# Performance work log

Hardware: AMD Instinct MI355X
Metric: run time of the kernel (lower is better)

The kernel has to match this reference:

```python
import jax, jax.numpy as jnp
import numpy as np

EMBED_DIM = 768
NUM_HEADS = 12
HEAD_DIM = EMBED_DIM // NUM_HEADS


def setup_inputs() -> dict:
    key = jax.random.key(0)
    k_x, k_wqkv, k_bqkv, k_wp, k_bp = jax.random.split(key, 5)
    B, N, C = 2, 2048, EMBED_DIM
    lim_qkv = 1.0 / np.sqrt(C)
    lim_p = 1.0 / np.sqrt(C)
    return {
        "x": jax.random.normal(k_x, (B, N, C), dtype=jnp.float32),
        # torch Linear weights: [out_features, in_features]
        "w_qkv": jax.random.uniform(k_wqkv, (3 * C, C), minval=-lim_qkv, maxval=lim_qkv, dtype=jnp.float32),
        "b_qkv": jax.random.uniform(k_bqkv, (3 * C,), minval=-lim_qkv, maxval=lim_qkv, dtype=jnp.float32),
        "w_proj": jax.random.uniform(k_wp, (C, C), minval=-lim_p, maxval=lim_p, dtype=jnp.float32),
        "b_proj": jax.random.uniform(k_bp, (C,), minval=-lim_p, maxval=lim_p, dtype=jnp.float32),
    }


def reference(x, w_qkv, b_qkv, w_proj, b_proj):
    b, n, c = x.shape
    h, d = NUM_HEADS, HEAD_DIM
    qkv = x @ w_qkv.T + b_qkv                      # [b, n, 3c]
    qkv = qkv.reshape(b, n, 3, h, d).transpose(2, 0, 3, 1, 4)  # [3, b, h, n, d]
    q, k, v = qkv[0], qkv[1], qkv[2]
    scale = d ** -0.5
    attn = jnp.einsum('bhnd,bhmd->bhnm', q, k) * scale  # [b, h, n, n]
    attn = jax.nn.softmax(attn, axis=-1)
    # dropout is identity at inference (eval mode)
    out = jnp.einsum('bhnm,bhmd->bhnd', attn, v)        # [b, h, n, d]
    out = out.transpose(0, 2, 1, 3).reshape(b, n, c)    # [b, n, c]
    return out @ w_proj.T + b_proj
```

## Files before the change

### kernel.cpp

```cpp
#include <hip/hip_runtime.h>
#include <cstdint>
#include <cstddef>

using u16    = uint16_t;
using u16x4  = __attribute__((ext_vector_type(4))) uint16_t;
using u16x8  = __attribute__((ext_vector_type(8))) uint16_t;
using bf16x2 = __attribute__((ext_vector_type(2))) __bf16;
using bf16x8 = __attribute__((ext_vector_type(8))) __bf16;
using f32x4  = __attribute__((ext_vector_type(4))) float;

__device__ __forceinline__ u16 f2b(float f) {
    union { float f; uint32_t u; } x; x.f = f;
    uint32_t r = x.u + 0x7FFFu + ((x.u >> 16) & 1u);
    return (u16)(r >> 16);
}
__device__ __forceinline__ uint32_t pk2(float a, float b) {
    bf16x2 t; t[0] = (__bf16)a; t[1] = (__bf16)b;
    return __builtin_bit_cast(uint32_t, t);
}
__device__ __forceinline__ bf16x8 ld8(const u16* p) {
    union { u16x8 v; u16x4 h[2]; } r;
    r.h[0] = *(const u16x4*)p;
    r.h[1] = *(const u16x4*)(p + 4);
    return __builtin_bit_cast(bf16x8, r.v);
}
__device__ __forceinline__ void st8(u16* p, u16x8 v) {
    union { u16x8 v; u16x4 h[2]; } r; r.v = v;
    *(u16x4*)p       = r.h[0];
    *(u16x4*)(p + 4) = r.h[1];
}

__device__ __forceinline__ void load16_async(const u16* g, u16* lds_base) {
    __builtin_amdgcn_global_load_lds(
        (const __attribute__((address_space(1))) u16*)g,
        (__attribute__((address_space(3))) u16*)(uint32_t)(uintptr_t)lds_base,
        16, 0, 0);
}

__global__ void conv_k(const float* __restrict__ x,  u16* __restrict__ xb,  int nx4,
                       const float* __restrict__ w1, u16* __restrict__ w1b, int n14,
                       const float* __restrict__ w2, u16* __restrict__ w2b, int n24)
{
    const int t   = blockIdx.x * blockDim.x + threadIdx.x;
    const int stp = gridDim.x * blockDim.x;
    for (int i = t; i < nx4; i += stp) {
        f32x4 v = ((const f32x4*)x)[i];
        u16x4 o;
        #pragma unroll
        for (int e = 0; e < 4; e++) o[e] = f2b(v[e]);
        ((u16x4*)xb)[i] = o;
    }
    for (int i = t; i < n14; i += stp) {
        f32x4 v = ((const f32x4*)w1)[i];
        u16x4 o;
        #pragma unroll
        for (int e = 0; e < 4; e++) o[e] = f2b(v[e]);
        ((u16x4*)w1b)[i] = o;
    }
    for (int i = t; i < n24; i += stp) {
        f32x4 v = ((const f32x4*)w2)[i];
        u16x4 o;
        #pragma unroll
        for (int e = 0; e < 4; e++) o[e] = f2b(v[e]);
        ((u16x4*)w2b)[i] = o;
    }
}

__global__ __launch_bounds__(256, 2) void gemm_qkv(
    const u16* __restrict__ A, const u16* __restrict__ W,
    const float* __restrict__ bias,
    u16* __restrict__ O0, u16* __restrict__ O1, u16* __restrict__ O2)
{
    __shared__ alignas(16) u16 As[128 * 32];
    __shared__ alignas(16) u16 Bs[128 * 32];
    const int tid  = threadIdx.x;
    const int wid  = tid >> 6, lane = tid & 63;
    const int quad = lane >> 4, lc = lane & 15;
    const int row0 = blockIdx.x * 128, col0 = blockIdx.y * 128;
    const int wm   = (wid >> 1) * 64, wn = (wid & 1) * 64;

    const int srA = wid * 32 + (lane >> 2);
    const int scA = (lane & 3) * 8;

    f32x4 acc[4][4] = {};

    for (int k0 = 0; k0 < 768; k0 += 32) {
        __syncthreads();
        #pragma unroll
        for (int t = 0; t < 2; t++) {
            load16_async(&A[(row0 + srA + t*16) * 768 + k0 + scA], &As[wid*1024 + t*512]);
            load16_async(&W[(col0 + srA + t*16) * 768 + k0 + scA], &Bs[wid*1024 + t*512]);
        }
        __syncthreads();

        bf16x8 a[4], b[4];
        #pragma unroll
        for (int i = 0; i < 4; i++)
            a[i] = __builtin_bit_cast(bf16x8, *(const u16x8*)&As[(wm + i*16 + lc)*32 + quad*8]);
        #pragma unroll
        for (int j = 0; j < 4; j++)
            b[j] = __builtin_bit_cast(bf16x8, *(const u16x8*)&Bs[(wn + j*16 + lc)*32 + quad*8]);
        #pragma unroll
        for (int i = 0; i < 4; i++)
            #pragma unroll
            for (int j = 0; j < 4; j++)
                acc[i][j] = __builtin_amdgcn_mfma_f32_16x16x32_bf16(a[i], b[j], acc[i][j], 0, 0, 0);
    }

    #pragma unroll
    for (int i = 0; i < 4; i++) {
        #pragma unroll
        for (int j = 0; j < 4; j++) {
            const int gc = col0 + wn + j*16 + lc;
            const float bv = bias[gc];
            #pragma unroll
            for (int r = 0; r < 4; r++) {
                const int gr = row0 + wm + i*16 + quad*4 + r;
                const u16 ob = f2b(acc[i][j][r] + bv);
                const int which = gc / 768;
                const int c2 = gc - which * 768;
                if (which == 0)      O0[gr * 768 + c2] = ob;
                else if (which == 1) O1[gr * 768 + c2] = ob;
                else {
                    const int hh = c2 >> 6, dd = c2 & 63;
                    const int bb = gr >> 11, nn = gr & 2047;
                    O2[((bb*12 + hh)*64 + dd)*2048 + nn] = ob;
                }
            }
        }
    }
}

__global__ __launch_bounds__(256, 4) void gemm_proj(
    const u16* __restrict__ A, const u16* __restrict__ W,
    const float* __restrict__ bias, float* __restrict__ F0)
{
    __shared__ alignas(16) u16 As[64 * 32];
    __shared__ alignas(16) u16 Bs[64 * 32];
    const int tid  = threadIdx.x;
    const int wid  = tid >> 6, lane = tid & 63;
    const int quad = lane >> 4, lc = lane & 15;
    const int row0 = blockIdx.x * 64, col0 = blockIdx.y * 64;
    const int wm   = (wid >> 1) * 32, wn = (wid & 1) * 32;

    const int srA = wid * 16 + (lane >> 2);
    const int scA = (lane & 3) * 8;

    f32x4 acc[2][2] = {};

    for (int k0 = 0; k0 < 768; k0 += 32) {
        __syncthreads();
        load16_async(&A[(row0 + srA) * 768 + k0 + scA], &As[wid*512]);
        load16_async(&W[(col0 + srA) * 768 + k0 + scA], &Bs[wid*512]);
        __syncthreads();

        bf16x8 a[2], b[2];
        #pragma unroll
        for (int i = 0; i < 2; i++)
            a[i] = __builtin_bit_cast(bf16x8, *(const u16x8*)&As[(wm + i*16 + lc)*32 + quad*8]);
        #pragma unroll
        for (int j = 0; j < 2; j++)
            b[j] = __builtin_bit_cast(bf16x8, *(const u16x8*)&Bs[(wn + j*16 + lc)*32 + quad*8]);
        #pragma unroll
        for (int i = 0; i < 2; i++)
            #pragma unroll
            for (int j = 0; j < 2; j++)
                acc[i][j] = __builtin_amdgcn_mfma_f32_16x16x32_bf16(a[i], b[j], acc[i][j], 0, 0, 0);
    }

    #pragma unroll
    for (int i = 0; i < 2; i++)
        #pragma unroll
        for (int j = 0; j < 2; j++) {
            const int gc = col0 + wn + j*16 + lc;
            const float bv = bias[gc];
            #pragma unroll
            for (int r = 0; r < 4; r++) {
                const int gr = row0 + wm + i*16 + quad*4 + r;
                F0[gr * 768 + gc] = acc[i][j][r] + bv;
            }
        }
}

__global__ __launch_bounds__(256, 2) void attn_k(
    const u16* __restrict__ Q, const u16* __restrict__ K,
    const u16* __restrict__ V, u16* __restrict__ O)
{
    __shared__ alignas(16) char lds[53760];
    u16* Ks = (u16*)(lds);
    u16* Vs = (u16*)(lds + 17408);
    u16* Ps = (u16*)(lds + 35328);
    float* Obuf = (float*)(lds);
    float* Lbuf = (float*)(lds + 35328);

    const int tid  = threadIdx.x;
    const int wid  = tid >> 6, lane = tid & 63;
    const int quad = lane >> 4, lc = lane & 15;
    const int li = blockIdx.x;
    const int bh = li >> 5, qt = li & 31;
    const int b = bh / 12, h = bh - b * 12;
    const int q0 = qt * 64;

    const u16* Qp = Q + ((size_t)b * 2048) * 768 + h * 64;
    const u16* Kp = K + ((size_t)b * 2048) * 768 + h * 64;
    const u16* Vp = V + (size_t)bh * 64 * 2048;
    u16*       Op = O + ((size_t)b * 2048) * 768 + h * 64;

    bf16x8 qf[4][2];
    #pragma unroll
    for (int qg = 0; qg < 4; qg++)
        #pragma unroll
        for (int kb = 0; kb < 2; kb++) {
            u16x8 t = *(const u16x8*)&Qp[(q0 + qg*16 + lc) * 768 + kb*32 + quad*8];
            bf16x8 sc;
            #pragma unroll
            for (int e = 0; e < 8; e++) {
                union { uint32_t u; float f; } z; z.u = ((uint32_t)t[e]) << 16;
                sc[e] = (__bf16)(z.f * 0.125f);
            }
            qf[qg][kb] = sc;
        }

    float l_[4] = {};
    f32x4 o_[4][4] = {};

    const int kr = tid >> 3, kseg = (tid & 7) * 8;
    const int vr = tid >> 4, vseg = (tid & 15) * 8;
    const int kb0 = wid * 32;

    u16x8 kpre[4], vpre[4];
    #pragma unroll
    for (int p = 0; p < 4; p++)
        kpre[p] = *(const u16x8*)&Kp[(kr + p*32)*768 + kseg];
    #pragma unroll
    for (int p = 0; p < 4; p++)
        vpre[p] = *(const u16x8*)&Vp[(vr + p*16)*2048 + vseg];

    for (int kt = 0; kt < 16; kt++) {
        __syncthreads();
        #pragma unroll
        for (int p = 0; p < 4; p++)
            st8(&Ks[(kr + p*32)*68 + kseg], kpre[p]);
        #pragma unroll
        for (int p = 0; p < 4; p++)
            st8(&Vs[(vr + p*16)*140 + vseg], vpre[p]);
        __syncthreads();

        if (kt < 15) {
            #pragma unroll
            for (int p = 0; p < 4; p++)
                kpre[p] = *(const u16x8*)&Kp[((kt+1)*128 + kr + p*32)*768 + kseg];
            #pragma unroll
            for (int p = 0; p < 4; p++)
                vpre[p] = *(const u16x8*)&Vp[(vr + p*16)*2048 + (kt+1)*128 + vseg];
        }

        f32x4 s[2][4] = {};
        #pragma unroll
        for (int g = 0; g < 2; g++) {
            bf16x8 k0f = ld8(&Ks[(kb0 + g*16 + lc)*68 + quad*8]);
            bf16x8 k1f = ld8(&Ks[(kb0 + g*16 + lc)*68 + 32 + quad*8]);
            #pragma unroll
            for (int qg = 0; qg < 4; qg++) {
                s[g][qg] = __builtin_amdgcn_mfma_f32_16x16x32_bf16(k0f, qf[qg][0], s[g][qg], 0, 0, 0);
                s[g][qg] = __builtin_amdgcn_mfma_f32_16x16x32_bf16(k1f, qf[qg][1], s[g][qg], 0, 0, 0);
            }
        }

        #pragma unroll
        for (int g = 0; g < 2; g++)
            #pragma unroll
            for (int qg = 0; qg < 4; qg++)
                #pragma unroll
                for (int r = 0; r < 4; r++) {
                    float p = __expf(s[g][qg][r]);
                    s[g][qg][r] = p;
                    l_[qg] += p;
                }

        #pragma unroll
        for (int g = 0; g < 2; g++)
            #pragma unroll
            for (int qg = 0; qg < 4; qg++) {
                uint2 w;
                w.x = pk2(s[g][qg][0], s[g][qg][1]);
                w.y = pk2(s[g][qg][2], s[g][qg][3]);
                *(uint2*)&Ps[(wid*64 + qg*16 + lc)*36 + g*16 + quad*4] = w;
            }

        bf16x8 pf[4], vf[4];
        #pragma unroll
        for (int qg = 0; qg < 4; qg++)
            pf[qg] = ld8(&Ps[(wid*64 + qg*16 + lc)*36 + quad*8]);
        #pragma unroll
        for (int dg = 0; dg < 4; dg++)
            vf[dg] = ld8(&Vs[(dg*16 + lc)*140 + kb0 + quad*8]);
        #pragma unroll
        for (int dg = 0; dg < 4; dg++)
            #pragma unroll
            for (int qg = 0; qg < 4; qg++)
                o_[dg][qg] = __builtin_amdgcn_mfma_f32_16x16x32_bf16(vf[dg], pf[qg], o_[dg][qg], 0, 0, 0);
    }

    #pragma unroll
    for (int qg = 0; qg < 4; qg++) {
        l_[qg] += __shfl_xor(l_[qg], 16);
        l_[qg] += __shfl_xor(l_[qg], 32);
    }
    __syncthreads();
    if (quad == 0)
        #pragma unroll
        for (int qg = 0; qg < 4; qg++)
            Lbuf[wid*64 + qg*16 + lc] = l_[qg];
    __syncthreads();

    const int eq = tid & 63;
    const int ed = (tid >> 6) * 8;
    const float linv = 1.0f / (Lbuf[0*64 + eq] + Lbuf[1*64 + eq] +
                               Lbuf[2*64 + eq] + Lbuf[3*64 + eq]);

    #pragma unroll
    for (int dh = 0; dh < 2; dh++) {
        __syncthreads();
        #pragma unroll
        for (int b2 = 0; b2 < 2; b2++) {
            const int dg = dh*2 + b2;
            #pragma unroll
            for (int qg = 0; qg < 4; qg++)
                #pragma unroll
                for (int r = 0; r < 4; r++)
                    Obuf[(wid*32 + b2*16 + quad*4 + r)*64 + qg*16 + lc] = o_[dg][qg][r];
        }
        __syncthreads();
        u16x8 ov;
        #pragma unroll
        for (int j = 0; j < 8; j++) {
            const float sum = Obuf[(0*32 + ed + j)*64 + eq] + Obuf[(1*32 + ed + j)*64 + eq] +
                              Obuf[(2*32 + ed + j)*64 + eq] + Obuf[(3*32 + ed + j)*64 + eq];
            ov[j] = f2b(sum * linv);
        }
        *(u16x8*)&Op[(size_t)(q0 + eq) * 768 + dh*32 + ed] = ov;
    }
}

extern "C" void kernel_launch(void* const* d_in, const int* in_sizes, int n_in,
                              void* d_out, int out_size, void* d_ws, size_t ws_size,
                              hipStream_t stream)
{
    const float* x    = (const float*)d_in[0];
    const float* wqkv = (const float*)d_in[1];
    const float* bqkv = (const float*)d_in[2];
    const float* wp   = (const float*)d_in[3];
    const float* bp   = (const float*)d_in[4];
    float* out = (float*)d_out;
    char* ws = (char*)d_ws;

    u16* Qw    = (u16*)(ws);
    u16* Vt    = (u16*)(ws + 6291456);
    u16* wqkvb = (u16*)(ws + 12582912);
    u16* wpb   = (u16*)(ws + 16121856);
    u16* Kw    = (u16*)d_out;
    u16* xb    = (u16*)((char*)d_out + 6291456);

    conv_k<<<512, 256, 0, stream>>>(x, xb, 3145728/4, wqkv, wqkvb, 1769472/4, wp, wpb, 589824/4);
    gemm_qkv<<<dim3(32, 18), 256, 0, stream>>>(xb, wqkvb, bqkv, Qw, Kw, Vt);
    attn_k<<<768, 256, 0, stream>>>(Qw, Kw, Vt, Qw);
    gemm_proj<<<dim3(64, 12), 256, 0, stream>>>(Qw, wpb, bp, out);
}
```

Before: 166.9 us.

## Register-prefetch GEMM tiles with padded LDS rows instead of direct global-to-LDS loads

Both projection GEMMs drop the global_load_lds async copies. Each thread now loads the next K-slice into registers while MFMAs run on the current LDS tile, then writes it to LDS after the barrier. LDS rows are padded from 32 to 40 elements to avoid bank conflicts on the fragment reads. The qkv kernel's occupancy hint rises from 2 to 3 blocks. The trade-off is more registers per thread and extra VGPR-to-LDS store instructions.

```diff
diff --git a/kernel.cpp b/kernel.cpp
--- a/kernel.cpp
+++ b/kernel.cpp
@@ -30,13 +30,6 @@
     *(u16x4*)(p + 4) = r.h[1];
 }
 
-__device__ __forceinline__ void load16_async(const u16* g, u16* lds_base) {
-    __builtin_amdgcn_global_load_lds(
-        (const __attribute__((address_space(1))) u16*)g,
-        (__attribute__((address_space(3))) u16*)(uint32_t)(uintptr_t)lds_base,
-        16, 0, 0);
-}
-
 __global__ void conv_k(const float* __restrict__ x,  u16* __restrict__ xb,  int nx4,
                        const float* __restrict__ w1, u16* __restrict__ w1b, int n14,
                        const float* __restrict__ w2, u16* __restrict__ w2b, int n24)
@@ -66,40 +59,55 @@
     }
 }
 
-__global__ __launch_bounds__(256, 2) void gemm_qkv(
+__global__ __launch_bounds__(256, 3) void gemm_qkv(
     const u16* __restrict__ A, const u16* __restrict__ W,
     const float* __restrict__ bias,
     u16* __restrict__ O0, u16* __restrict__ O1, u16* __restrict__ O2)
 {
-    __shared__ alignas(16) u16 As[128 * 32];
-    __shared__ alignas(16) u16 Bs[128 * 32];
+    __shared__ alignas(16) u16 As[128 * 40];
+    __shared__ alignas(16) u16 Bs[128 * 40];
     const int tid  = threadIdx.x;
     const int wid  = tid >> 6, lane = tid & 63;
     const int quad = lane >> 4, lc = lane & 15;
     const int row0 = blockIdx.x * 128, col0 = blockIdx.y * 128;
     const int wm   = (wid >> 1) * 64, wn = (wid & 1) * 64;
 
-    const int srA = wid * 32 + (lane >> 2);
-    const int scA = (lane & 3) * 8;
+    const int sr = wid * 32 + (lane >> 2);
+    const int sc = (lane & 3) * 8;
 
     f32x4 acc[4][4] = {};
 
+    u16x8 apre[2], wpre[2];
+    #pragma unroll
+    for (int t = 0; t < 2; t++) {
+        apre[t] = *(const u16x8*)&A[(row0 + sr + t*16) * 768 + sc];
+        wpre[t] = *(const u16x8*)&W[(col0 + sr + t*16) * 768 + sc];
+    }
+
     for (int k0 = 0; k0 < 768; k0 += 32) {
         __syncthreads();
         #pragma unroll
         for (int t = 0; t < 2; t++) {
-            load16_async(&A[(row0 + srA + t*16) * 768 + k0 + scA], &As[wid*1024 + t*512]);
-            load16_async(&W[(col0 + srA + t*16) * 768 + k0 + scA], &Bs[wid*1024 + t*512]);
-        }
-        __syncthreads();
+            *(u16x8*)&As[(sr + t*16)*40 + sc] = apre[t];
+            *(u16x8*)&Bs[(sr + t*16)*40 + sc] = wpre[t];
+        }
+        __syncthreads();
+
+        if (k0 < 736) {
+            #pragma unroll
+            for (int t = 0; t < 2; t++) {
+                apre[t] = *(const u16x8*)&A[(row0 + sr + t*16) * 768 + k0 + 32 + sc];
+                wpre[t] = *(const u16x8*)&W[(col0 + sr + t*16) * 768 + k0 + 32 + sc];
+            }
+        }
 
         bf16x8 a[4], b[4];
         #pragma unroll
         for (int i = 0; i < 4; i++)
-            a[i] = __builtin_bit_cast(bf16x8, *(const u16x8*)&As[(wm + i*16 + lc)*32 + quad*8]);
+            a[i] = __builtin_bit_cast(bf16x8, *(const u16x8*)&As[(wm + i*16 + lc)*40 + quad*8]);
         #pragma unroll
         for (int j = 0; j < 4; j++)
-            b[j] = __builtin_bit_cast(bf16x8, *(const u16x8*)&Bs[(wn + j*16 + lc)*32 + quad*8]);
+            b[j] = __builtin_bit_cast(bf16x8, *(const u16x8*)&Bs[(wn + j*16 + lc)*40 + quad*8]);
         #pragma unroll
         for (int i = 0; i < 4; i++)
             #pragma unroll
@@ -135,32 +143,41 @@
     const u16* __restrict__ A, const u16* __restrict__ W,
     const float* __restrict__ bias, float* __restrict__ F0)
 {
-    __shared__ alignas(16) u16 As[64 * 32];
-    __shared__ alignas(16) u16 Bs[64 * 32];
+    __shared__ alignas(16) u16 As[64 * 40];
+    __shared__ alignas(16) u16 Bs[64 * 40];
     const int tid  = threadIdx.x;
     const int wid  = tid >> 6, lane = tid & 63;
     const int quad = lane >> 4, lc = lane & 15;
     const int row0 = blockIdx.x * 64, col0 = blockIdx.y * 64;
     const int wm   = (wid >> 1) * 32, wn = (wid & 1) * 32;
 
-    const int srA = wid * 16 + (lane >> 2);
-    const int scA = (lane & 3) * 8;
+    const int sr = wid * 16 + (lane >> 2);
+    const int sc = (lane & 3) * 8;
 
     f32x4 acc[2][2] = {};
 
+    u16x8 apre, wpre;
+    apre = *(const u16x8*)&A[(row0 + sr) * 768 + sc];
+    wpre = *(const u16x8*)&W[(col0 + sr) * 768 + sc];
+
     for (int k0 = 0; k0 < 768; k0 += 32) {
         __syncthreads();
-        load16_async(&A[(row0 + srA) * 768 + k0 + scA], &As[wid*512]);
-        load16_async(&W[(col0 + srA) * 768 + k0 + scA], &Bs[wid*512]);
-        __syncthreads();
+        *(u16x8*)&As[sr*40 + sc] = apre;
+        *(u16x8*)&Bs[sr*40 + sc] = wpre;
+        __syncthreads();
+
+        if (k0 < 736) {
+            apre = *(const u16x8*)&A[(row0 + sr) * 768 + k0 + 32 + sc];
+            wpre = *(const u16x8*)&W[(col0 + sr) * 768 + k0 + 32 + sc];
+        }
 
         bf16x8 a[2], b[2];
         #pragma unroll
         for (int i = 0; i < 2; i++)
-            a[i] = __builtin_bit_cast(bf16x8, *(const u16x8*)&As[(wm + i*16 + lc)*32 + quad*8]);
+            a[i] = __builtin_bit_cast(bf16x8, *(const u16x8*)&As[(wm + i*16 + lc)*40 + quad*8]);
         #pragma unroll
         for (int j = 0; j < 2; j++)
-            b[j] = __builtin_bit_cast(bf16x8, *(const u16x8*)&Bs[(wn + j*16 + lc)*32 + quad*8]);
+            b[j] = __builtin_bit_cast(bf16x8, *(const u16x8*)&Bs[(wn + j*16 + lc)*40 + quad*8]);
         #pragma unroll
         for (int i = 0; i < 2; i++)
             #pragma unroll
```

Result: slower. 171.6 us (+2.8%).
